# Optimization experiments

Measured on AMD Instinct MI355X. Metric: run time of the kernel, lower is better.

## Reference

```python
import jax, jax.numpy as jnp
import numpy as np
import math

B, C_IN, C_OUT, H, W = 16, 128, 128, 56, 56
K, S, P, D = 3, 1, 1, 1
PROD_KS = K * K


def _unfold(x, k, s, p, d):
    # torch.nn.functional.unfold equivalent -> (B, k*k, C, Ho*Wo)
    b, c, h, w = x.shape
    ho = (h + 2 * p - d * (k - 1) - 1) // s + 1
    wo = (w + 2 * p - d * (k - 1) - 1) // s + 1
    xp = jnp.pad(x, ((0, 0), (0, 0), (p, p), (p, p)))
    patches = [
        xp[:, :, i * d: i * d + (ho - 1) * s + 1: s, j * d: j * d + (wo - 1) * s + 1: s]
        for i in range(k) for j in range(k)
    ]
    u = jnp.stack(patches, axis=1)  # (B, K2, C, Ho, Wo)
    return u.reshape(b, k * k, c, ho * wo), ho, wo


def setup_inputs() -> dict:
    key = jax.random.key(0)
    k1, k2, k3, k4 = jax.random.split(key, 4)
    stdv = 1.0 / math.sqrt(C_IN * PROD_KS)
    x = jax.random.normal(k1, (B, C_IN, H, W), dtype=jnp.float32)
    weight = jax.random.uniform(k2, (1, PROD_KS, C_OUT, C_IN), dtype=jnp.float32,
                                minval=-stdv, maxval=stdv)
    b_k = jax.random.uniform(k3, (1, PROD_KS, 1, C_OUT, 1), dtype=jnp.float32,
                             minval=-stdv, maxval=stdv)
    bias = jax.random.uniform(k4, (C_OUT,), dtype=jnp.float32, minval=-stdv, maxval=stdv)
    return {"x": x, "weight": weight, "b_k": b_k, "bias": bias}


def reference(x, weight, b_k, bias):
    batch = x.shape[0]
    u, ho, wo = _unfold(x, K, S, P, D)          # (B, K2, C_in, L)
    inpt = u.transpose(0, 1, 3, 2)               # (B, K2, L, C_in)
    # GEMM: (B,K2,L,Cin) x (K2,Cout,Cin) -> (B,K2,L,Cout)
    out = jnp.einsum('bklc,koc->bklo', inpt, weight[0])
    bk = b_k[0, :, 0, :, 0]                      # (K2, Cout)
    # fused cos/sin contraction over kernel positions -> (B, L, Cout) each
    a = jnp.einsum('bklo,ko->blo', out, jnp.cos(bk))
    bb = jnp.einsum('bklo,ko->blo', out, jnp.sin(bk))
    eps = 1e-05
    a_gt = a > 0
    b_gt = bb > 0
    ab_eq = a_gt == b_gt
    theta = jnp.where(ab_eq, jnp.arctan(bb / (a + eps)), -jnp.arctan(a / (bb + eps)))
    pi = math.pi
    peak = jnp.where(ab_eq & a_gt, pi / 2.0,
           jnp.where(ab_eq & ~a_gt, -pi / 2.0,
           jnp.where(~ab_eq & ~b_gt, -pi, 0.0)))
    theta = peak - theta
    o = jnp.sin(theta) * a + jnp.cos(theta) * bb  # (B, L, Cout)
    o = o.transpose(0, 2, 1) + bias[None, :, None]  # (B, Cout, L)
    conv_out = o.reshape(batch, C_OUT, ho, wo)
    theta_out = (theta / pi).transpose(0, 2, 1).reshape(batch, C_OUT, ho, wo)
    return jnp.concatenate([conv_out, theta_out], axis=1)
```

## Files before the change

### kernel.cpp

```cpp
#include <hip/hip_runtime.h>
#include <hip/hip_bf16.h>
#include <math.h>

#define NB   16
#define CIN  128
#define COUT 128
#define HH   56
#define WW   56
#define LL   3136

typedef __attribute__((ext_vector_type(8))) short short8;
typedef __attribute__((ext_vector_type(16))) float f32x16;
typedef __attribute__((ext_vector_type(4))) float f32x4;
typedef __attribute__((ext_vector_type(4))) unsigned int uint4v;

#define PXT    256
#define NPXT   13
#define XC     58
#define XPLANE 7424
#define XUSH   14848
#define XUNITS 1856
#define XHALF  928
#define WUSH   18432
#define WBYTES 36864
#define WUNITS 2304


#define XT_ROWS 62
#define XT_PLANE_USH (XT_ROWS*XC*16)
#define XT_CG_STRIDE 3682304

#define CSD_OFF 256
#define WSP_OFF 32768
#define XT_OFF  1212416
#define XT_SIZE 29458432
#define WL_OFF  (XT_OFF + XT_SIZE)

__global__ void prep_kernel(const float* __restrict__ w, const float* __restrict__ bk,
                            const float* __restrict__ x,
                            double* __restrict__ csd, unsigned short* __restrict__ wsp,
                            unsigned short* __restrict__ xt, unsigned* __restrict__ cnt) {
    int bid = blockIdx.x;
    if (bid == 0 && threadIdx.x == 0) *cnt = 0u;
    if (bid < 576) {
        int i = bid * 256 + threadIdx.x;
        if (i >= 9*COUT*CIN) return;
        int k = i / (COUT*CIN);
        int rem = i - k*(COUT*CIN);
        int oc = rem >> 7, c = rem & 127;
        float bkv = bk[k*COUT + oc];
        if (c == 0) {
            double bd = (double)bkv;
            csd[k*COUT + oc]          = cos(bd);
            csd[9*COUT + k*COUT + oc] = sin(bd);
        }
        float ck = cosf(bkv), sk = sinf(bkv);
        float wv = w[i];
        float fa = ck * wv;
        float fb = sk * wv;
        __hip_bfloat16 ah = __float2bfloat16(fa);
        __hip_bfloat16 al = __float2bfloat16(fa - __bfloat162float(ah));
        __hip_bfloat16 bh = __float2bfloat16(fb);
        __hip_bfloat16 bl = __float2bfloat16(fb - __bfloat162float(bh));
        int ocb = oc >> 5;
        int rowa = oc & 31;
        int cg = c >> 4, cp = c & 15;
        int lane = rowa + ((cp >> 3) << 5);
        int bp = cp & 7;
        size_t img = ((size_t)ocb*8 + cg) * WUSH;
        wsp[img + (size_t)((k*4+0)*64 + lane)*8 + bp] = *(unsigned short*)&ah;
        wsp[img + (size_t)((k*4+1)*64 + lane)*8 + bp] = *(unsigned short*)&bh;
        wsp[img + (size_t)((k*4+2)*64 + lane)*8 + bp] = *(unsigned short*)&al;
        wsp[img + (size_t)((k*4+3)*64 + lane)*8 + bp] = *(unsigned short*)&bl;
    } else {
        int i = (bid - 576) * 256 + threadIdx.x;
        if (i < 100352) {
            int c4 = i % 14; int t = i / 14;
            int row1 = t % 56; t /= 56;
            int bat = t & 15, cg = t >> 4;
            const float* xp = x + ((size_t)(bat*CIN + cg*16))*LL + row1*WW + c4*4;
            unsigned short hi[4][16], lo[4][16];
            #pragma unroll
            for (int j = 0; j < 16; j++) {
                f32x4 v = *(const f32x4*)(xp + (size_t)j*LL);
                #pragma unroll
                for (int cc = 0; cc < 4; cc++) {
                    float f = v[cc];
                    __hip_bfloat16 h = __float2bfloat16(f);
                    __hip_bfloat16 l = __float2bfloat16(f - __bfloat162float(h));
                    hi[cc][j] = *(unsigned short*)&h;
                    lo[cc][j] = *(unsigned short*)&l;
                }
            }
            size_t base = ((((size_t)cg*16 + bat)*2 + 0)*XT_ROWS + (row1+1))*XC + (c4*4 + 1);
            #pragma unroll
            for (int cc = 0; cc < 4; cc++) {
                unsigned short* dh = xt + (base + cc)*16;
                unsigned short* dl = dh + XT_PLANE_USH;
                *(uint4v*)dh       = *(const uint4v*)&hi[cc][0];
                *(uint4v*)(dh + 8) = *(const uint4v*)&hi[cc][8];
                *(uint4v*)dl       = *(const uint4v*)&lo[cc][0];
                *(uint4v*)(dl + 8) = *(const uint4v*)&lo[cc][8];
            }
        } else if (i < 218112) {
            int i2 = i - 100352;
            int unit = i2 % 460; int t = i2 / 460;
            int pl = t & 1; t >>= 1;
            int bat = t & 15, cg = t >> 4;
            int row, c58;
            if (unit < 348) {
                int zr = unit / 58; c58 = unit - zr*58;
                row = (zr == 0) ? 0 : (56 + zr);
            } else {
                int u2 = unit - 348; row = 1 + (u2 >> 1); c58 = (u2 & 1) ? 57 : 0;
            }
            size_t base = ((((size_t)cg*16 + bat)*2 + pl)*XT_ROWS + row)*XC + c58;
            uint4v zz = {0u,0u,0u,0u};
            *(uint4v*)(xt + base*16)     = zz;
            *(uint4v*)(xt + base*16 + 8) = zz;
        }
    }
}

__global__ __launch_bounds__(256, 2)
void mfma_kernel(const unsigned short* __restrict__ xt, const unsigned short* __restrict__ wsp,
                 const float* __restrict__ bias, float* __restrict__ out,
                 unsigned* __restrict__ cnt, unsigned* __restrict__ wl, unsigned cap)
{
    __shared__ __align__(16) unsigned short SMX[XUSH];
    __shared__ __align__(16) unsigned short SMW[WUSH];
    __shared__ float sm_bias[32];

    const int tid = threadIdx.x;
    int bid = blockIdx.x;
    int wk = (bid & 7) * 104 + (bid >> 3);
    const int ocb = wk & 3; wk >>= 2;
    const int pxt = wk % NPXT;
    const int bat = wk / NPXT;
    const int l0  = pxt * PXT;
    const int o0  = ocb * 32;
    const int yf  = l0 / WW;

    const int lane = tid & 63;
    const int n    = lane & 31;
    const int kh   = lane >> 5;
    const int wave = tid >> 6;

    if (tid < 32) sm_bias[tid] = bias[o0 + tid];

    unsigned xoff[8];
    #pragma unroll
    for (int k = 0; k < 8; k++) {
        int u = tid + 256*k;
        int uc = u < XUNITS ? u : XUNITS-1;
        int pl = uc >= XHALF ? 1 : 0;
        int rem = uc - pl*XHALF;
        int q  = rem >> 1;
        int hl = rem & 1;
        int hg = hl ^ ((q >> 2) & 1);
        int r  = q / XC;
        int c  = q - r*XC;
        xoff[k] = (unsigned)((((bat*2 + pl)*XT_ROWS + (yf + r))*XC + c)*32 + hg*16);
    }

    int q0g[2];
    #pragma unroll
    for (int g = 0; g < 2; g++) {
        int p  = l0 + wave*64 + g*32 + n;
        int pc = p < LL ? p : LL-1;
        int py = pc / WW, pxx = pc - py*WW;
        q0g[g] = (py - yf)*XC + pxx;
    }

    f32x16 acc_a[2], acc_b[2];
    #pragma unroll
    for (int g = 0; g < 2; g++) {
        #pragma unroll
        for (int r = 0; r < 16; r++) { acc_a[g][r] = 0.f; acc_b[g][r] = 0.f; }
    }

    const char* xtB  = (const char*)xt;
    const char* wspB = (const char*)wsp + (size_t)ocb * (8*(size_t)WBYTES);

    auto stage_x = [&](int chn) {
        const char* xp = xtB + (size_t)chn * XT_CG_STRIDE;
        #pragma unroll
        for (int k = 0; k < 7; k++) {
            __builtin_amdgcn_global_load_lds(
                (const __attribute__((address_space(1))) unsigned int*)(xp + xoff[k]),
                (__attribute__((address_space(3))) unsigned int*)&SMX[(wave*64 + 256*k)*8],
                16, 0, 0);
        }
        if (wave == 0)
            __builtin_amdgcn_global_load_lds(
                (const __attribute__((address_space(1))) unsigned int*)(xp + xoff[7]),
                (__attribute__((address_space(3))) unsigned int*)&SMX[1792*8],
                16, 0, 0);
    };
    auto stage_w = [&](int chn) {
        const char* wp = wspB + (size_t)chn * (size_t)WBYTES;
        #pragma unroll
        for (int k = 0; k < 9; k++) {
            __builtin_amdgcn_global_load_lds(
                (const __attribute__((address_space(1))) unsigned int*)(wp + (tid + 256*k)*16),
                (__attribute__((address_space(3))) unsigned int*)&SMW[(wave*64 + 256*k)*8],
                16, 0, 0);
        }
    };

    stage_x(0);
    stage_w(0);
    __syncthreads();

    const unsigned short* awp = &SMW[lane*8];

    #pragma unroll 1
    for (int ch = 0; ch < 8; ch++) {
        #pragma unroll
        for (int tap = 0; tap < 9; tap++) {
            const int ky = tap / 3, kx = tap - 3*ky;
            short8 Aha = *(const short8*)&awp[(tap*4+0)*512];
            short8 Ahb = *(const short8*)&awp[(tap*4+1)*512];
            short8 Ala = *(const short8*)&awp[(tap*4+2)*512];
            short8 Alb = *(const short8*)&awp[(tap*4+3)*512];
            __builtin_amdgcn_s_setprio(1);
            #pragma unroll
            for (int g = 0; g < 2; g++) {
                int q  = q0g[g] + ky*XC + kx;
                int si = q*16 + ((kh ^ ((q>>2)&1)) << 3);
                short8 Bh = *(const short8*)&SMX[si];
                short8 Bl = *(const short8*)&SMX[XPLANE + si];
                acc_a[g] = __builtin_amdgcn_mfma_f32_32x32x16_bf16(Ala, Bh, acc_a[g], 0,0,0);
                acc_a[g] = __builtin_amdgcn_mfma_f32_32x32x16_bf16(Aha, Bl, acc_a[g], 0,0,0);
                acc_a[g] = __builtin_amdgcn_mfma_f32_32x32x16_bf16(Aha, Bh, acc_a[g], 0,0,0);
                acc_b[g] = __builtin_amdgcn_mfma_f32_32x32x16_bf16(Alb, Bh, acc_b[g], 0,0,0);
                acc_b[g] = __builtin_amdgcn_mfma_f32_32x32x16_bf16(Ahb, Bl, acc_b[g], 0,0,0);
                acc_b[g] = __builtin_amdgcn_mfma_f32_32x32x16_bf16(Ahb, Bh, acc_b[g], 0,0,0);
            }
            __builtin_amdgcn_s_setprio(0);
        }
        if (ch < 7) {
            __syncthreads();
            stage_x(ch+1);
            stage_w(ch+1);
            __syncthreads();
        }
    }

    const float eps = 1e-05f;
    const float PIf = 3.14159265358979323846f;
    size_t obase = (size_t)bat * (2*COUT) * LL;

    #pragma unroll
    for (int g = 0; g < 2; g++) {
        const int pcol = wave*64 + g*32 + n;
        const int pp = l0 + pcol;
        #pragma unroll
        for (int r = 0; r < 16; r++) {
            int row = (r & 3) + 8*(r >> 2) + 4*kh;
            float av = acc_a[g][r];
            float bv = acc_b[g][r];
            bool flag = (pp < LL) &&
                        (fabsf(av) < 1.5e-4f || (bv < 1.05e-5f && bv > -2.05e-5f));
            unsigned long long m = __ballot(flag);
            if (m) {
                int leader = (int)__ffsll((long long)m) - 1;
                unsigned base = 0;
                if (lane == leader) base = atomicAdd(cnt, (unsigned)__popcll(m));
                base = __shfl(base, leader);
                if (flag) {
                    unsigned slot = base + (unsigned)__popcll(m & ((1ULL << lane) - 1ULL));
                    if (slot < cap)
                        wl[slot] = ((unsigned)(bat*LL + pp) << 7) | (unsigned)(o0 + row);
                }
            }
            bool ag = av > 0.f, bg = bv > 0.f;
            bool eq = (ag == bg);
            float ratio = eq ? (bv / (av + eps)) : (av / (bv + eps));
            float at = atanf(ratio);
            float peak = eq ? (ag ? PIf*0.5f : -PIf*0.5f) : (bg ? 0.0f : -PIf);
            float th = peak - (eq ? at : -at);
            float c = 1.0f / sqrtf(1.0f + ratio*ratio);
            float t = eq ? (av + ratio*bv) : (ratio*av + bv);
            bool pos = eq ? ag : bg;
            float o = (pos ? c : -c) * t;
            if (pp < LL) {
                out[obase + (size_t)(o0+row)*LL + pp]      = o + sm_bias[row];
                out[obase + (size_t)(COUT+o0+row)*LL + pp] = th * (1.0f/PIf);
            }
        }
    }
}

__global__ __launch_bounds__(256)
void fixup_kernel(const float* __restrict__ x, const float* __restrict__ w,
                  const double* __restrict__ csd, const float* __restrict__ bias,
                  const unsigned* __restrict__ cnt, const unsigned* __restrict__ wl,
                  unsigned cap, float* __restrict__ out) {
    const int lane   = threadIdx.x & 63;
    const int waveid = (blockIdx.x * 256 + threadIdx.x) >> 6;
    const int nwaves = gridDim.x * 4;
    unsigned nf = *cnt; if (nf > cap) nf = cap;
    const double PI = 3.14159265358979323846;

    for (unsigned u = waveid; u < nf; u += nwaves) {
        unsigned idx = wl[u];
        int oc = idx & 127;
        unsigned rest = idx >> 7;
        int bb_ = rest / LL;
        int l   = rest - bb_*LL;
        int yy  = l / WW;
        int xx  = l - yy*WW;
        const float* xb = x + (size_t)bb_ * CIN * LL;

        double pa = 0.0, pb = 0.0;
        #pragma unroll
        for (int k = 0; k < 9; k++) {
            int dy = k/3, dx = k - dy*3;
            int py = yy + dy - 1, px = xx + dx - 1;
            double pk = 0.0;
            if ((unsigned)py < HH && (unsigned)px < WW) {
                int base = py*WW + px;
                const float* wr = w + k*(COUT*CIN) + oc*CIN;
                int c = lane;
                pk  = (double)xb[(size_t)c*LL + base] * (double)wr[c];
                c = lane + 64;
                pk += (double)xb[(size_t)c*LL + base] * (double)wr[c];
            }
            pa += csd[k*COUT + oc] * pk;
            pb += csd[9*COUT + k*COUT + oc] * pk;
        }
        #pragma unroll
        for (int off = 32; off > 0; off >>= 1) {
            pa += __shfl_xor(pa, off, 64);
            pb += __shfl_xor(pb, off, 64);
        }
        if (lane == 0) {
            bool ag = pa > 0.0, bg = pb > 0.0;
            bool eq = (ag == bg);
            double th;
            if (eq) th = (ag ? PI*0.5 : -PI*0.5) - atan(pb / (pa + 1e-5));
            else    th = (bg ? 0.0 : -PI) + atan(pa / (pb + 1e-5));
            double o = sin(th)*pa + cos(th)*pb + (double)bias[oc];
            out[((size_t)bb_*(2*COUT) + oc) * LL + l]        = (float)o;
            out[((size_t)bb_*(2*COUT) + COUT + oc) * LL + l] = (float)(th / PI);
        }
    }
}

extern "C" void kernel_launch(void* const* d_in, const int* in_sizes, int n_in,
                              void* d_out, int out_size, void* d_ws, size_t ws_size,
                              hipStream_t stream) {
    const float* x    = (const float*)d_in[0];
    const float* w    = (const float*)d_in[1];
    const float* bk   = (const float*)d_in[2];
    const float* bias = (const float*)d_in[3];
    float* out = (float*)d_out;

    char* ws = (char*)d_ws;
    unsigned*       cnt = (unsigned*)ws;
    double*         csd = (double*)(ws + CSD_OFF);
    unsigned short* wsp = (unsigned short*)(ws + WSP_OFF);
    unsigned short* xt  = (unsigned short*)(ws + XT_OFF);
    unsigned*       wl  = (unsigned*)(ws + WL_OFF);
    unsigned cap = (ws_size > (size_t)WL_OFF + 4096) ? (unsigned)((ws_size - WL_OFF) / 4) : 0u;

    hipLaunchKernelGGL(prep_kernel,  dim3(1428), dim3(256), 0, stream,
                       w, bk, x, csd, wsp, xt, cnt);
    hipLaunchKernelGGL(mfma_kernel,  dim3(NB*NPXT*4), dim3(256), 0, stream,
                       xt, wsp, bias, out, cnt, wl, cap);
    hipLaunchKernelGGL(fixup_kernel, dim3(256), dim3(256), 0, stream,
                       x, w, csd, bias, cnt, wl, cap, out);
}
```

Before: 338.4 us.

## Pack cos and sin weight rows into one MFMA tile per block

The cos- and sin-weighted weights for 16 output channels are now stacked into a single 32-row MFMA A operand, so each block keeps one accumulator pair instead of separate a/b accumulators. Blocks now cover 16 output channels, so the grid doubles to 8 channel groups, the weight LDS tile halves, and launch bounds rise to 3 blocks per CU. The goal is fewer registers and less LDS per block, giving more occupancy and latency hiding. The cost is that every input tile is staged by twice as many blocks, which doubles X traffic from L2 and LDS staging work.

```diff
diff --git a/kernel.cpp b/kernel.cpp
--- a/kernel.cpp
+++ b/kernel.cpp
@@ -21,9 +21,9 @@
 #define XUSH   14848
 #define XUNITS 1856
 #define XHALF  928
-#define WUSH   18432
-#define WBYTES 36864
-#define WUNITS 2304
+#define WUSH   9216
+#define WBYTES 18432
+#define WUNITS 1152
 
 
 #define XT_ROWS 62
@@ -62,16 +62,17 @@
         __hip_bfloat16 al = __float2bfloat16(fa - __bfloat162float(ah));
         __hip_bfloat16 bh = __float2bfloat16(fb);
         __hip_bfloat16 bl = __float2bfloat16(fb - __bfloat162float(bh));
-        int ocb = oc >> 5;
-        int rowa = oc & 31;
+        int ocb = oc >> 4;
+        int row_a = oc & 15;
         int cg = c >> 4, cp = c & 15;
-        int lane = rowa + ((cp >> 3) << 5);
+        int lane_a = row_a + ((cp >> 3) << 5);
+        int lane_b = 16 + row_a + ((cp >> 3) << 5);
         int bp = cp & 7;
         size_t img = ((size_t)ocb*8 + cg) * WUSH;
-        wsp[img + (size_t)((k*4+0)*64 + lane)*8 + bp] = *(unsigned short*)&ah;
-        wsp[img + (size_t)((k*4+1)*64 + lane)*8 + bp] = *(unsigned short*)&bh;
-        wsp[img + (size_t)((k*4+2)*64 + lane)*8 + bp] = *(unsigned short*)&al;
-        wsp[img + (size_t)((k*4+3)*64 + lane)*8 + bp] = *(unsigned short*)&bl;
+        wsp[img + (size_t)((k*2+0)*64 + lane_a)*8 + bp] = *(unsigned short*)&ah;
+        wsp[img + (size_t)((k*2+0)*64 + lane_b)*8 + bp] = *(unsigned short*)&bh;
+        wsp[img + (size_t)((k*2+1)*64 + lane_a)*8 + bp] = *(unsigned short*)&al;
+        wsp[img + (size_t)((k*2+1)*64 + lane_b)*8 + bp] = *(unsigned short*)&bl;
     } else {
         int i = (bid - 576) * 256 + threadIdx.x;
         if (i < 100352) {
@@ -122,23 +123,23 @@
     }
 }
 
-__global__ __launch_bounds__(256, 2)
+__global__ __launch_bounds__(256, 3)
 void mfma_kernel(const unsigned short* __restrict__ xt, const unsigned short* __restrict__ wsp,
                  const float* __restrict__ bias, float* __restrict__ out,
                  unsigned* __restrict__ cnt, unsigned* __restrict__ wl, unsigned cap)
 {
     __shared__ __align__(16) unsigned short SMX[XUSH];
     __shared__ __align__(16) unsigned short SMW[WUSH];
-    __shared__ float sm_bias[32];
+    __shared__ float sm_bias[16];
 
     const int tid = threadIdx.x;
     int bid = blockIdx.x;
-    int wk = (bid & 7) * 104 + (bid >> 3);
-    const int ocb = wk & 3; wk >>= 2;
+    int wk = (bid & 7) * 208 + (bid >> 3);
+    const int ocb = wk & 7; wk >>= 3;
     const int pxt = wk % NPXT;
     const int bat = wk / NPXT;
     const int l0  = pxt * PXT;
-    const int o0  = ocb * 32;
+    const int o0  = ocb * 16;
     const int yf  = l0 / WW;
 
     const int lane = tid & 63;
@@ -146,7 +147,7 @@
     const int kh   = lane >> 5;
     const int wave = tid >> 6;
 
-    if (tid < 32) sm_bias[tid] = bias[o0 + tid];
+    if (tid < 16) sm_bias[tid] = bias[o0 + tid];
 
     unsigned xoff[8];
     #pragma unroll
@@ -172,11 +173,11 @@
         q0g[g] = (py - yf)*XC + pxx;
     }
 
-    f32x16 acc_a[2], acc_b[2];
+    f32x16 acc[2];
     #pragma unroll
     for (int g = 0; g < 2; g++) {
         #pragma unroll
-        for (int r = 0; r < 16; r++) { acc_a[g][r] = 0.f; acc_b[g][r] = 0.f; }
+        for (int r = 0; r < 16; r++) acc[g][r] = 0.f;
     }
 
     const char* xtB  = (const char*)xt;
@@ -200,12 +201,17 @@
     auto stage_w = [&](int chn) {
         const char* wp = wspB + (size_t)chn * (size_t)WBYTES;
         #pragma unroll
-        for (int k = 0; k < 9; k++) {
+        for (int k = 0; k < 4; k++) {
             __builtin_amdgcn_global_load_lds(
                 (const __attribute__((address_space(1))) unsigned int*)(wp + (tid + 256*k)*16),
                 (__attribute__((address_space(3))) unsigned int*)&SMW[(wave*64 + 256*k)*8],
                 16, 0, 0);
         }
+        if (wave < 2)
+            __builtin_amdgcn_global_load_lds(
+                (const __attribute__((address_space(1))) unsigned int*)(wp + (1024 + tid)*16),
+                (__attribute__((address_space(3))) unsigned int*)&SMW[(1024 + wave*64)*8],
+                16, 0, 0);
     };
 
     stage_x(0);
@@ -219,10 +225,8 @@
         #pragma unroll
         for (int tap = 0; tap < 9; tap++) {
             const int ky = tap / 3, kx = tap - 3*ky;
-            short8 Aha = *(const short8*)&awp[(tap*4+0)*512];
-            short8 Ahb = *(const short8*)&awp[(tap*4+1)*512];
-            short8 Ala = *(const short8*)&awp[(tap*4+2)*512];
-            short8 Alb = *(const short8*)&awp[(tap*4+3)*512];
+            short8 Ah = *(const short8*)&awp[(tap*2+0)*512];
+            short8 Al = *(const short8*)&awp[(tap*2+1)*512];
             __builtin_amdgcn_s_setprio(1);
             #pragma unroll
             for (int g = 0; g < 2; g++) {
@@ -230,12 +234,9 @@
                 int si = q*16 + ((kh ^ ((q>>2)&1)) << 3);
                 short8 Bh = *(const short8*)&SMX[si];
                 short8 Bl = *(const short8*)&SMX[XPLANE + si];
-                acc_a[g] = __builtin_amdgcn_mfma_f32_32x32x16_bf16(Ala, Bh, acc_a[g], 0,0,0);
-                acc_a[g] = __builtin_amdgcn_mfma_f32_32x32x16_bf16(Aha, Bl, acc_a[g], 0,0,0);
-                acc_a[g] = __builtin_amdgcn_mfma_f32_32x32x16_bf16(Aha, Bh, acc_a[g], 0,0,0);
-                acc_b[g] = __builtin_amdgcn_mfma_f32_32x32x16_bf16(Alb, Bh, acc_b[g], 0,0,0);
-                acc_b[g] = __builtin_amdgcn_mfma_f32_32x32x16_bf16(Ahb, Bl, acc_b[g], 0,0,0);
-                acc_b[g] = __builtin_amdgcn_mfma_f32_32x32x16_bf16(Ahb, Bh, acc_b[g], 0,0,0);
+                acc[g] = __builtin_amdgcn_mfma_f32_32x32x16_bf16(Al, Bh, acc[g], 0,0,0);
+                acc[g] = __builtin_amdgcn_mfma_f32_32x32x16_bf16(Ah, Bl, acc[g], 0,0,0);
+                acc[g] = __builtin_amdgcn_mfma_f32_32x32x16_bf16(Ah, Bh, acc[g], 0,0,0);
             }
             __builtin_amdgcn_s_setprio(0);
         }
@@ -256,10 +257,10 @@
         const int pcol = wave*64 + g*32 + n;
         const int pp = l0 + pcol;
         #pragma unroll
-        for (int r = 0; r < 16; r++) {
-            int row = (r & 3) + 8*(r >> 2) + 4*kh;
-            float av = acc_a[g][r];
-            float bv = acc_b[g][r];
+        for (int r = 0; r < 8; r++) {
+            int row16 = (r & 3) + 8*(r >> 2) + 4*kh;
+            float av = acc[g][r];
+            float bv = acc[g][r+8];
             bool flag = (pp < LL) &&
                         (fabsf(av) < 1.5e-4f || (bv < 1.05e-5f && bv > -2.05e-5f));
             unsigned long long m = __ballot(flag);
@@ -271,7 +272,7 @@
                 if (flag) {
                     unsigned slot = base + (unsigned)__popcll(m & ((1ULL << lane) - 1ULL));
                     if (slot < cap)
-                        wl[slot] = ((unsigned)(bat*LL + pp) << 7) | (unsigned)(o0 + row);
+                        wl[slot] = ((unsigned)(bat*LL + pp) << 7) | (unsigned)(o0 + row16);
                 }
             }
             bool ag = av > 0.f, bg = bv > 0.f;
@@ -285,8 +286,8 @@
             bool pos = eq ? ag : bg;
             float o = (pos ? c : -c) * t;
             if (pp < LL) {
-                out[obase + (size_t)(o0+row)*LL + pp]      = o + sm_bias[row];
-                out[obase + (size_t)(COUT+o0+row)*LL + pp] = th * (1.0f/PIf);
+                out[obase + (size_t)(o0+row16)*LL + pp]      = o + sm_bias[row16];
+                out[obase + (size_t)(COUT+o0+row16)*LL + pp] = th * (1.0f/PIf);
             }
         }
     }
@@ -367,7 +368,7 @@
 
     hipLaunchKernelGGL(prep_kernel,  dim3(1428), dim3(256), 0, stream,
                        w, bk, x, csd, wsp, xt, cnt);
-    hipLaunchKernelGGL(mfma_kernel,  dim3(NB*NPXT*4), dim3(256), 0, stream,
+    hipLaunchKernelGGL(mfma_kernel,  dim3(NB*NPXT*8), dim3(256), 0, stream,
                        xt, wsp, bias, out, cnt, wl, cap);
     hipLaunchKernelGGL(fixup_kernel, dim3(256), dim3(256), 0, stream,
                        x, w, csd, bias, cnt, wl, cap, out);
```

Result: faster. 326.8 us (-3.4%).
